# Kernel optimization log

Hardware: AMD Instinct MI355X
Metric: run time of the kernel (lower is better)

## Reference

```python
import jax, jax.numpy as jnp
import numpy as np

NUM_LAYERS = 3
HIDDEN = 128
EDGE_CH = 4
VOCAB = 100
N_NODES = 100000
N_EDGES = 600000


def setup_inputs() -> dict:
    key = jax.random.key(0)
    ks = jax.random.split(key, 10)
    z = jax.random.randint(ks[0], (N_NODES,), 0, VOCAB)
    edge_index = jax.random.randint(ks[1], (2, N_EDGES), 0, N_NODES)
    edge_attr = jax.random.normal(ks[2], (N_EDGES, EDGE_CH), dtype=jnp.float32)
    batch_vec = jnp.sort(jax.random.randint(ks[3], (N_NODES,), 0, 512))
    s = 1.0 / np.sqrt(HIDDEN)
    emb = jax.random.normal(ks[4], (VOCAB, HIDDEN), dtype=jnp.float32)
    We = jax.random.normal(ks[5], (NUM_LAYERS, EDGE_CH, HIDDEN), dtype=jnp.float32) * 0.5
    be = jnp.zeros((NUM_LAYERS, HIDDEN), dtype=jnp.float32)
    W1 = jax.random.normal(ks[6], (NUM_LAYERS, HIDDEN, HIDDEN), dtype=jnp.float32) * s
    b1 = jnp.zeros((NUM_LAYERS, HIDDEN), dtype=jnp.float32)
    W2 = jax.random.normal(ks[7], (NUM_LAYERS, HIDDEN, HIDDEN), dtype=jnp.float32) * s
    b2 = jnp.zeros((NUM_LAYERS, HIDDEN), dtype=jnp.float32)
    return {"emb": emb, "We": We, "be": be, "W1": W1, "b1": b1,
            "W2": W2, "b2": b2, "edge_attr": edge_attr,
            "z": z, "edge_index": edge_index, "batch_vec": batch_vec}


def reference(emb, We, be, W1, b1, W2, b2, edge_attr, z, edge_index, batch_vec):
    # atom embedding lookup: [N, H]
    x = emb[z]
    src, dst = edge_index[0], edge_index[1]
    n = x.shape[0]
    for l in range(NUM_LAYERS):
        # edge feature projection: [E, H]
        e = edge_attr @ We[l] + be[l]
        # GINE message: relu(x_j + e_ij), gather over src nodes
        m = jax.nn.relu(x[src] + e)
        # scatter-sum aggregation to destination nodes
        agg = jax.ops.segment_sum(m, dst, num_segments=n)
        # (1 + eps) * x + agg, eps = 0, then 2-layer MLP with silu act
        h = x + agg
        x = jax.nn.silu(h @ W1[l] + b1[l]) @ W2[l] + b2[l]
    return (x, batch_vec)
```

## Files before the change

kernel.cpp:

```cpp
#include <hip/hip_runtime.h>
#include <hip/hip_fp16.h>
#include <math.h>

#define N_NODES 100000
#define N_EDGES 600000
#define HIDDEN 128
#define EDGE_CH 4
#define NUM_LAYERS 3
#define MLP_ROWS 64

#define SCAN_BLOCK 256
#define SCAN_GRID ((N_NODES + SCAN_BLOCK - 1) / SCAN_BLOCK)

#define HSTR 132
#define MLP3_TILES ((N_NODES + 127) / 128)
#define MLP3_GRID 256

typedef short bf16x8 __attribute__((ext_vector_type(8)));
typedef float f32x4  __attribute__((ext_vector_type(4)));

__device__ inline unsigned short f2bf(float x) {
    unsigned u = __float_as_uint(x);
    return (unsigned short)((u + 0x7fff + ((u >> 16) & 1)) >> 16);
}
__device__ inline float bf2f(unsigned short b) { return __uint_as_float(((unsigned)b) << 16); }

__device__ inline float4 h8tof4(uint2 u) {
    __half2 a = *reinterpret_cast<const __half2*>(&u.x);
    __half2 b = *reinterpret_cast<const __half2*>(&u.y);
    float2 fa = __half22float2(a);
    float2 fb = __half22float2(b);
    return make_float4(fa.x, fa.y, fb.x, fb.y);
}
__device__ inline uint2 f4toh8(float4 v) {
    __half2 a = __floats2half2_rn(v.x, v.y);
    __half2 b = __floats2half2_rn(v.z, v.w);
    uint2 u;
    u.x = *reinterpret_cast<unsigned*>(&a);
    u.y = *reinterpret_cast<unsigned*>(&b);
    return u;
}


__global__ void embed_init_kernel(const float* __restrict__ emb,
                                  const int* __restrict__ z,
                                  float* __restrict__ x,
                                  float* __restrict__ agg,
                                  int write_agg,
                                  __half* __restrict__ xh,
                                  int write_xh) {
    int t = blockIdx.x * blockDim.x + threadIdx.x;
    int node = t >> 5;
    int c4 = t & 31;
    if (node < N_NODES) {
        float4 v = ((const float4*)(emb + (size_t)z[node] * HIDDEN))[c4];
        ((float4*)(x + (size_t)node * HIDDEN))[c4] = v;
        if (write_agg)
            ((float4*)(agg + (size_t)node * HIDDEN))[c4] = v;
        if (write_xh)
            ((uint2*)(xh + (size_t)node * HIDDEN))[c4] = f4toh8(v);
    }
}

__global__ void wprep_kernel(const float* __restrict__ W1, const float* __restrict__ W2,
                             unsigned short* __restrict__ wt) {
    int idx = blockIdx.x * blockDim.x + threadIdx.x;
    if (idx >= NUM_LAYERS * 2 * HIDDEN * HIDDEN) return;
    int j    = idx & 7;
    int lane = (idx >> 3) & 63;
    int ks   = (idx >> 9) & 3;
    int nt   = (idx >> 11) & 7;
    int mat  = (idx >> 14) & 1;
    int l    = idx >> 15;
    int n = nt * 16 + (lane & 15);
    int k = ks * 32 + (lane >> 4) * 8 + j;
    const float* W = mat ? W2 : W1;
    wt[idx] = f2bf(W[(size_t)l * HIDDEN * HIDDEN + (size_t)k * HIDDEN + n]);
}

__global__ __launch_bounds__(512, 1) void mlp_mfma3_kernel(
        const float* __restrict__ h,
        const unsigned short* __restrict__ wfrag,
        const float* __restrict__ b1, const float* __restrict__ b2,
        float* __restrict__ x,
        __half* __restrict__ xh,
        int write_xh) {
    __shared__ short wlds[2 * 16384];
    __shared__ float tbuf[8 * 16 * HSTR];
    int tid   = threadIdx.x;
    int wave  = tid >> 6;
    int lane  = tid & 63;
    int row16 = lane & 15;
    int quad  = lane >> 4;
    float* myt = tbuf + wave * 16 * HSTR;

    for (int i = tid; i < 4096; i += 512)
        ((float4*)wlds)[i] = ((const float4*)wfrag)[i];
    __syncthreads();

    float bias1[8], bias2[8];
    #pragma unroll
    for (int nt = 0; nt < 8; nt++) {
        bias1[nt] = b1[nt * 16 + row16];
        bias2[nt] = b2[nt * 16 + row16];
    }

    for (int tile = blockIdx.x; tile < MLP3_TILES; tile += gridDim.x) {
        int wnode0 = tile * 128 + wave * 16;
        int mnode  = wnode0 + row16;
        bool valid = (mnode < N_NODES);
        const float* hrow = h + (size_t)(valid ? mnode : 0) * HIDDEN + quad * 8;

        bf16x8 ahi[4], alo[4];
        #pragma unroll
        for (int ks = 0; ks < 4; ks++) {
            float v[8];
            *(float4*)(v + 0) = valid ? *(const float4*)(hrow + ks * 32 + 0) : make_float4(0.f,0.f,0.f,0.f);
            *(float4*)(v + 4) = valid ? *(const float4*)(hrow + ks * 32 + 4) : make_float4(0.f,0.f,0.f,0.f);
            bf16x8 hi, lo;
            #pragma unroll
            for (int j = 0; j < 8; j++) {
                unsigned short hb = f2bf(v[j]);
                hi[j] = (short)hb;
                lo[j] = (short)f2bf(v[j] - bf2f(hb));
            }
            ahi[ks] = hi; alo[ks] = lo;
        }

        f32x4 acc[8];
        #pragma unroll
        for (int nt = 0; nt < 8; nt++) acc[nt] = (f32x4){0.f, 0.f, 0.f, 0.f};
        #pragma unroll
        for (int ks = 0; ks < 4; ks++) {
            #pragma unroll
            for (int nt = 0; nt < 8; nt++) {
                bf16x8 Bv = *(const bf16x8*)(wlds + (size_t)((nt * 4 + ks) * 64 + lane) * 8);
                acc[nt] = __builtin_amdgcn_mfma_f32_16x16x32_bf16(ahi[ks], Bv, acc[nt], 0, 0, 0);
                acc[nt] = __builtin_amdgcn_mfma_f32_16x16x32_bf16(alo[ks], Bv, acc[nt], 0, 0, 0);
            }
        }

        #pragma unroll
        for (int nt = 0; nt < 8; nt++) {
            #pragma unroll
            for (int r = 0; r < 4; r++) {
                float v = acc[nt][r] + bias1[nt];
                v = v / (1.f + __expf(-v));
                myt[(quad * 4 + r) * HSTR + nt * 16 + row16] = v;
            }
        }

        #pragma unroll
        for (int ks = 0; ks < 4; ks++) {
            const float* p = myt + row16 * HSTR + ks * 32 + quad * 8;
            float v[8];
            *(float4*)(v + 0) = *(const float4*)(p + 0);
            *(float4*)(v + 4) = *(const float4*)(p + 4);
            bf16x8 hi, lo;
            #pragma unroll
            for (int j = 0; j < 8; j++) {
                unsigned short hb = f2bf(v[j]);
                hi[j] = (short)hb;
                lo[j] = (short)f2bf(v[j] - bf2f(hb));
            }
            ahi[ks] = hi; alo[ks] = lo;
        }

        #pragma unroll
        for (int nt = 0; nt < 8; nt++) acc[nt] = (f32x4){0.f, 0.f, 0.f, 0.f};
        #pragma unroll
        for (int ks = 0; ks < 4; ks++) {
            #pragma unroll
            for (int nt = 0; nt < 8; nt++) {
                bf16x8 Bv = *(const bf16x8*)(wlds + (size_t)(16384 + ((nt * 4 + ks) * 64 + lane) * 8));
                acc[nt] = __builtin_amdgcn_mfma_f32_16x16x32_bf16(ahi[ks], Bv, acc[nt], 0, 0, 0);
                acc[nt] = __builtin_amdgcn_mfma_f32_16x16x32_bf16(alo[ks], Bv, acc[nt], 0, 0, 0);
            }
        }

        #pragma unroll
        for (int nt = 0; nt < 8; nt++) {
            #pragma unroll
            for (int r = 0; r < 4; r++) {
                int node = wnode0 + quad * 4 + r;
                if (node < N_NODES) {
                    float v = acc[nt][r] + bias2[nt];
                    x[(size_t)node * HIDDEN + nt * 16 + row16] = v;
                    if (write_xh)
                        xh[(size_t)node * HIDDEN + nt * 16 + row16] = __float2half_rn(v);
                }
            }
        }
    }
}

__global__ void mlp_kernel(const float* __restrict__ h,
                           const float* __restrict__ W1, const float* __restrict__ b1,
                           const float* __restrict__ W2, const float* __restrict__ b2,
                           float* __restrict__ x) {
    __shared__ float hs[MLP_ROWS * HIDDEN];
    int rg = threadIdx.x >> 5;
    int c4 = threadIdx.x & 31;
    int node0 = blockIdx.x * MLP_ROWS;

    for (int i = threadIdx.x; i < MLP_ROWS * 32; i += 256) {
        int node = node0 + (i >> 5);
        float4 v = (node < N_NODES)
                 ? ((const float4*)(h + (size_t)node * HIDDEN))[i & 31]
                 : make_float4(0.f, 0.f, 0.f, 0.f);
        ((float4*)hs)[i] = v;
    }
    __syncthreads();

    float4 acc[8];
    {
        float4 bv = ((const float4*)b1)[c4];
        #pragma unroll
        for (int r = 0; r < 8; r++) acc[r] = bv;
    }
    const float* hbase = hs + rg * 8 * HIDDEN;

    for (int k4 = 0; k4 < HIDDEN; k4 += 4) {
        float4 w0 = ((const float4*)(W1 + (size_t)(k4 + 0) * HIDDEN))[c4];
        float4 w1 = ((const float4*)(W1 + (size_t)(k4 + 1) * HIDDEN))[c4];
        float4 w2 = ((const float4*)(W1 + (size_t)(k4 + 2) * HIDDEN))[c4];
        float4 w3 = ((const float4*)(W1 + (size_t)(k4 + 3) * HIDDEN))[c4];
        #pragma unroll
        for (int r = 0; r < 8; r++) {
            float4 hv = *(const float4*)(hbase + r * HIDDEN + k4);
            acc[r].x += hv.x*w0.x + hv.y*w1.x + hv.z*w2.x + hv.w*w3.x;
            acc[r].y += hv.x*w0.y + hv.y*w1.y + hv.z*w2.y + hv.w*w3.y;
            acc[r].z += hv.x*w0.z + hv.y*w1.z + hv.z*w2.z + hv.w*w3.z;
            acc[r].w += hv.x*w0.w + hv.y*w1.w + hv.z*w2.w + hv.w*w3.w;
        }
    }

    __syncthreads();
    #pragma unroll
    for (int r = 0; r < 8; r++) {
        float4 a = acc[r];
        a.x = a.x / (1.f + __expf(-a.x));
        a.y = a.y / (1.f + __expf(-a.y));
        a.z = a.z / (1.f + __expf(-a.z));
        a.w = a.w / (1.f + __expf(-a.w));
        *(float4*)(hs + (rg * 8 + r) * HIDDEN + c4 * 4) = a;
    }
    __syncthreads();

    {
        float4 bv = ((const float4*)b2)[c4];
        #pragma unroll
        for (int r = 0; r < 8; r++) acc[r] = bv;
    }
    for (int k4 = 0; k4 < HIDDEN; k4 += 4) {
        float4 w0 = ((const float4*)(W2 + (size_t)(k4 + 0) * HIDDEN))[c4];
        float4 w1 = ((const float4*)(W2 + (size_t)(k4 + 1) * HIDDEN))[c4];
        float4 w2 = ((const float4*)(W2 + (size_t)(k4 + 2) * HIDDEN))[c4];
        float4 w3 = ((const float4*)(W2 + (size_t)(k4 + 3) * HIDDEN))[c4];
        #pragma unroll
        for (int r = 0; r < 8; r++) {
            float4 hv = *(const float4*)(hbase + r * HIDDEN + k4);
            acc[r].x += hv.x*w0.x + hv.y*w1.x + hv.z*w2.x + hv.w*w3.x;
            acc[r].y += hv.x*w0.y + hv.y*w1.y + hv.z*w2.y + hv.w*w3.y;
            acc[r].z += hv.x*w0.z + hv.y*w1.z + hv.z*w2.z + hv.w*w3.z;
            acc[r].w += hv.x*w0.w + hv.y*w1.w + hv.z*w2.w + hv.w*w3.w;
        }
    }

    #pragma unroll
    for (int r = 0; r < 8; r++) {
        int node = node0 + rg * 8 + r;
        if (node < N_NODES)
            ((float4*)(x + (size_t)node * HIDDEN))[c4] = acc[r];
    }
}

__global__ void batch_out_kernel(const int* __restrict__ bv, float* __restrict__ out) {
    int i = blockIdx.x * blockDim.x + threadIdx.x;
    if (i < N_NODES) out[i] = (float)bv[i];
}


__global__ void zero_kernel(int* __restrict__ p, int n) {
    int i = blockIdx.x * blockDim.x + threadIdx.x;
    if (i < n) p[i] = 0;
}

__global__ void hist_kernel(const int* __restrict__ dst, int* __restrict__ cnt) {
    int e = blockIdx.x * blockDim.x + threadIdx.x;
    if (e < N_EDGES) atomicAdd(&cnt[dst[e]], 1);
}

__global__ void scan_partial_kernel(const int* __restrict__ cnt, int* __restrict__ bsum) {
    __shared__ int s[SCAN_BLOCK];
    int i = blockIdx.x * SCAN_BLOCK + threadIdx.x;
    s[threadIdx.x] = (i < N_NODES) ? cnt[i] : 0;
    __syncthreads();
    for (int off = SCAN_BLOCK / 2; off > 0; off >>= 1) {
        if (threadIdx.x < off) s[threadIdx.x] += s[threadIdx.x + off];
        __syncthreads();
    }
    if (threadIdx.x == 0) bsum[blockIdx.x] = s[0];
}

__global__ void scan_base_kernel(int* __restrict__ bsum) {
    __shared__ int s[512];
    int t = threadIdx.x;
    s[t] = (t < SCAN_GRID) ? bsum[t] : 0;
    __syncthreads();
    for (int off = 1; off < 512; off <<= 1) {
        int v = (t >= off) ? s[t - off] : 0;
        __syncthreads();
        s[t] += v;
        __syncthreads();
    }
    if (t < SCAN_GRID) bsum[t] = (t > 0) ? s[t - 1] : 0;
}

__global__ void scan_final_kernel(int* __restrict__ cnt, const int* __restrict__ bsum) {
    __shared__ int s[SCAN_BLOCK];
    int i = blockIdx.x * SCAN_BLOCK + threadIdx.x;
    int v = (i < N_NODES) ? cnt[i] : 0;
    s[threadIdx.x] = v;
    __syncthreads();
    for (int off = 1; off < SCAN_BLOCK; off <<= 1) {
        int u = (threadIdx.x >= off) ? s[threadIdx.x - off] : 0;
        __syncthreads();
        s[threadIdx.x] += u;
        __syncthreads();
    }
    if (i < N_NODES) cnt[i] = bsum[blockIdx.x] + s[threadIdx.x] - v;
}

__global__ void scatter2_kernel(const int* __restrict__ dst,
                                const int* __restrict__ src,
                                const float* __restrict__ edge_attr,
                                int* __restrict__ pos,
                                int* __restrict__ ssrc,
                                float4* __restrict__ sea) {
    int e = blockIdx.x * blockDim.x + threadIdx.x;
    if (e < N_EDGES) {
        int p = atomicAdd(&pos[dst[e]], 1);
        ssrc[p] = src[e];
        sea[p] = ((const float4*)edge_attr)[e];
    }
}

__global__ void gather2_kernel(const float* __restrict__ x,
                               const int* __restrict__ ssrc,
                               const float4* __restrict__ sea,
                               const int* __restrict__ pos,
                               const float* __restrict__ We_l,
                               const float* __restrict__ be_l,
                               float* __restrict__ h) {
    __shared__ float sWe[EDGE_CH * HIDDEN];
    __shared__ float sbe[HIDDEN];
    for (int i = threadIdx.x; i < EDGE_CH * HIDDEN; i += blockDim.x) sWe[i] = We_l[i];
    if (threadIdx.x < HIDDEN) sbe[threadIdx.x] = be_l[threadIdx.x];
    __syncthreads();

    int t = blockIdx.x * blockDim.x + threadIdx.x;
    int node = t >> 5;
    int c4 = t & 31;
    if (node >= N_NODES) return;

    int start = (node == 0) ? 0 : pos[node - 1];
    int end = pos[node];

    float4 w0 = ((const float4*)sWe)[0 * 32 + c4];
    float4 w1 = ((const float4*)sWe)[1 * 32 + c4];
    float4 w2 = ((const float4*)sWe)[2 * 32 + c4];
    float4 w3 = ((const float4*)sWe)[3 * 32 + c4];
    float4 bb = ((const float4*)sbe)[c4];

    float4 acc = make_float4(0.f, 0.f, 0.f, 0.f);
    int j = start;
    if (j < end) {
        int s0 = ssrc[j];
        float4 ea0 = sea[j];
        for (; j + 1 < end; j++) {
            int s1 = ssrc[j + 1];
            float4 ea1 = sea[j + 1];
            float4 xv = ((const float4*)(x + (size_t)s0 * HIDDEN))[c4];
            float m0 = xv.x + ea0.x*w0.x + ea0.y*w1.x + ea0.z*w2.x + ea0.w*w3.x + bb.x;
            float m1 = xv.y + ea0.x*w0.y + ea0.y*w1.y + ea0.z*w2.y + ea0.w*w3.y + bb.y;
            float m2 = xv.z + ea0.x*w0.z + ea0.y*w1.z + ea0.z*w2.z + ea0.w*w3.z + bb.z;
            float m3 = xv.w + ea0.x*w0.w + ea0.y*w1.w + ea0.z*w2.w + ea0.w*w3.w + bb.w;
            acc.x += fmaxf(m0, 0.f); acc.y += fmaxf(m1, 0.f);
            acc.z += fmaxf(m2, 0.f); acc.w += fmaxf(m3, 0.f);
            s0 = s1; ea0 = ea1;
        }
        float4 xv = ((const float4*)(x + (size_t)s0 * HIDDEN))[c4];
        float m0 = xv.x + ea0.x*w0.x + ea0.y*w1.x + ea0.z*w2.x + ea0.w*w3.x + bb.x;
        float m1 = xv.y + ea0.x*w0.y + ea0.y*w1.y + ea0.z*w2.y + ea0.w*w3.y + bb.y;
        float m2 = xv.z + ea0.x*w0.z + ea0.y*w1.z + ea0.z*w2.z + ea0.w*w3.z + bb.z;
        float m3 = xv.w + ea0.x*w0.w + ea0.y*w1.w + ea0.z*w2.w + ea0.w*w3.w + bb.w;
        acc.x += fmaxf(m0, 0.f); acc.y += fmaxf(m1, 0.f);
        acc.z += fmaxf(m2, 0.f); acc.w += fmaxf(m3, 0.f);
    }
    float4 xi = ((const float4*)(x + (size_t)node * HIDDEN))[c4];
    acc.x += xi.x; acc.y += xi.y; acc.z += xi.z; acc.w += xi.w;
    ((float4*)(h + (size_t)node * HIDDEN))[c4] = acc;
}

__global__ void gather3_kernel(const __half* __restrict__ xh,
                               const int* __restrict__ ssrc,
                               const float4* __restrict__ sea,
                               const int* __restrict__ pos,
                               const float* __restrict__ We_l,
                               const float* __restrict__ be_l,
                               float* __restrict__ h) {
    __shared__ float sWe[EDGE_CH * HIDDEN];
    __shared__ float sbe[HIDDEN];
    for (int i = threadIdx.x; i < EDGE_CH * HIDDEN; i += blockDim.x) sWe[i] = We_l[i];
    if (threadIdx.x < HIDDEN) sbe[threadIdx.x] = be_l[threadIdx.x];
    __syncthreads();

    int t = blockIdx.x * blockDim.x + threadIdx.x;
    int node = t >> 5;
    int c4 = t & 31;
    if (node >= N_NODES) return;

    int start = (node == 0) ? 0 : pos[node - 1];
    int end = pos[node];

    float4 w0 = ((const float4*)sWe)[0 * 32 + c4];
    float4 w1 = ((const float4*)sWe)[1 * 32 + c4];
    float4 w2 = ((const float4*)sWe)[2 * 32 + c4];
    float4 w3 = ((const float4*)sWe)[3 * 32 + c4];
    float4 bb = ((const float4*)sbe)[c4];

    float4 acc = make_float4(0.f, 0.f, 0.f, 0.f);
    int j = start;
    if (j < end) {
        int s0 = ssrc[j];
        float4 ea0 = sea[j];
        for (; j + 1 < end; j++) {
            int s1 = ssrc[j + 1];
            float4 ea1 = sea[j + 1];
            float4 xv = h8tof4(((const uint2*)(xh + (size_t)s0 * HIDDEN))[c4]);
            float m0 = xv.x + ea0.x*w0.x + ea0.y*w1.x + ea0.z*w2.x + ea0.w*w3.x + bb.x;
            float m1 = xv.y + ea0.x*w0.y + ea0.y*w1.y + ea0.z*w2.y + ea0.w*w3.y + bb.y;
            float m2 = xv.z + ea0.x*w0.z + ea0.y*w1.z + ea0.z*w2.z + ea0.w*w3.z + bb.z;
            float m3 = xv.w + ea0.x*w0.w + ea0.y*w1.w + ea0.z*w2.w + ea0.w*w3.w + bb.w;
            acc.x += fmaxf(m0, 0.f); acc.y += fmaxf(m1, 0.f);
            acc.z += fmaxf(m2, 0.f); acc.w += fmaxf(m3, 0.f);
            s0 = s1; ea0 = ea1;
        }
        float4 xv = h8tof4(((const uint2*)(xh + (size_t)s0 * HIDDEN))[c4]);
        float m0 = xv.x + ea0.x*w0.x + ea0.y*w1.x + ea0.z*w2.x + ea0.w*w3.x + bb.x;
        float m1 = xv.y + ea0.x*w0.y + ea0.y*w1.y + ea0.z*w2.y + ea0.w*w3.y + bb.y;
        float m2 = xv.z + ea0.x*w0.z + ea0.y*w1.z + ea0.z*w2.z + ea0.w*w3.z + bb.z;
        float m3 = xv.w + ea0.x*w0.w + ea0.y*w1.w + ea0.z*w2.w + ea0.w*w3.w + bb.w;
        acc.x += fmaxf(m0, 0.f); acc.y += fmaxf(m1, 0.f);
        acc.z += fmaxf(m2, 0.f); acc.w += fmaxf(m3, 0.f);
    }
    float4 xi = h8tof4(((const uint2*)(xh + (size_t)node * HIDDEN))[c4]);
    acc.x += xi.x; acc.y += xi.y; acc.z += xi.z; acc.w += xi.w;
    ((float4*)(h + (size_t)node * HIDDEN))[c4] = acc;
}


__global__ void edge_kernel(const float* __restrict__ x,
                            const float* __restrict__ edge_attr,
                            const int* __restrict__ src,
                            const int* __restrict__ dst,
                            const float* __restrict__ We_l,
                            const float* __restrict__ be_l,
                            float* __restrict__ agg) {
    __shared__ float sWe[EDGE_CH * HIDDEN];
    __shared__ float sbe[HIDDEN];
    for (int i = threadIdx.x; i < EDGE_CH * HIDDEN; i += blockDim.x) sWe[i] = We_l[i];
    if (threadIdx.x < HIDDEN) sbe[threadIdx.x] = be_l[threadIdx.x];
    __syncthreads();

    int t = blockIdx.x * blockDim.x + threadIdx.x;
    int e = t >> 5;
    if (e >= N_EDGES) return;
    int c4 = t & 31;

    int s = src[e];
    int d = dst[e];
    float4 ea = ((const float4*)edge_attr)[e];
    float4 w0 = ((const float4*)sWe)[0 * 32 + c4];
    float4 w1 = ((const float4*)sWe)[1 * 32 + c4];
    float4 w2 = ((const float4*)sWe)[2 * 32 + c4];
    float4 w3 = ((const float4*)sWe)[3 * 32 + c4];
    float4 bb = ((const float4*)sbe)[c4];
    float4 xv = ((const float4*)(x + (size_t)s * HIDDEN))[c4];

    float m0 = xv.x + ea.x*w0.x + ea.y*w1.x + ea.z*w2.x + ea.w*w3.x + bb.x;
    float m1 = xv.y + ea.x*w0.y + ea.y*w1.y + ea.z*w2.y + ea.w*w3.y + bb.y;
    float m2 = xv.z + ea.x*w0.z + ea.y*w1.z + ea.z*w2.z + ea.w*w3.z + bb.z;
    float m3 = xv.w + ea.x*w0.w + ea.y*w1.w + ea.z*w2.w + ea.w*w3.w + bb.w;

    float* ap = agg + (size_t)d * HIDDEN + c4 * 4;
    atomicAdd(ap + 0, fmaxf(m0, 0.f));
    atomicAdd(ap + 1, fmaxf(m1, 0.f));
    atomicAdd(ap + 2, fmaxf(m2, 0.f));
    atomicAdd(ap + 3, fmaxf(m3, 0.f));
}


extern "C" void kernel_launch(void* const* d_in, const int* in_sizes, int n_in,
                              void* d_out, int out_size, void* d_ws, size_t ws_size,
                              hipStream_t stream) {
    const float* emb       = (const float*)d_in[0];
    const float* We        = (const float*)d_in[1];
    const float* be        = (const float*)d_in[2];
    const float* W1        = (const float*)d_in[3];
    const float* b1        = (const float*)d_in[4];
    const float* W2        = (const float*)d_in[5];
    const float* b2        = (const float*)d_in[6];
    const float* edge_attr = (const float*)d_in[7];
    const int*   z         = (const int*)d_in[8];
    const int*   ei        = (const int*)d_in[9];
    const int*   bv        = (const int*)d_in[10];

    float* x   = (float*)d_out;
    float* agg = (float*)d_ws;
    const int* src = ei;
    const int* dst = ei + N_EDGES;

    const size_t AGG_BYTES  = (size_t)N_NODES * HIDDEN * sizeof(float);
    const size_t POS_BYTES  = (size_t)N_NODES * sizeof(int);
    const size_t SRC_BYTES  = (size_t)N_EDGES * sizeof(int);
    const size_t EA_BYTES   = (size_t)N_EDGES * 4 * sizeof(float);
    const size_t BSUM_BYTES = ((size_t)SCAN_GRID * sizeof(int) + 15) & ~15;
    const size_t WT_ELEMS   = (size_t)NUM_LAYERS * 2 * HIDDEN * HIDDEN;
    const size_t WT_BYTES   = WT_ELEMS * sizeof(unsigned short);
    const size_t XH_BYTES   = (size_t)N_NODES * HIDDEN * sizeof(__half);

    const size_t OFF_POS  = AGG_BYTES;
    const size_t OFF_SRC  = OFF_POS + POS_BYTES;
    const size_t OFF_EA   = OFF_SRC + SRC_BYTES;
    const size_t OFF_BSUM = OFF_EA + EA_BYTES;
    const size_t OFF_WT   = OFF_BSUM + BSUM_BYTES;
    const size_t OFF_XH   = OFF_WT + WT_BYTES;
    const size_t TOTAL    = OFF_WT + WT_BYTES;
    const size_t TOTAL2   = OFF_XH + XH_BYTES;

    const int MLP_GRID = (N_NODES + MLP_ROWS - 1) / MLP_ROWS;

    if (ws_size >= OFF_BSUM + BSUM_BYTES) {
        int*    pos  = (int*)((char*)d_ws + OFF_POS);
        int*    ssrc = (int*)((char*)d_ws + OFF_SRC);
        float4* sea  = (float4*)((char*)d_ws + OFF_EA);
        int*    bsum = (int*)((char*)d_ws + OFF_BSUM);
        const bool mfma  = (ws_size >= TOTAL);
        const bool halfx = (ws_size >= TOTAL2);
        unsigned short* wt = (unsigned short*)((char*)d_ws + OFF_WT);
        __half* xh = (__half*)((char*)d_ws + OFF_XH);

        embed_init_kernel<<<(N_NODES * 32) / 256, 256, 0, stream>>>(
            emb, z, x, agg, 0, xh, halfx ? 1 : 0);
        zero_kernel<<<(N_NODES + 255) / 256, 256, 0, stream>>>(pos, N_NODES);
        hist_kernel<<<(N_EDGES + 255) / 256, 256, 0, stream>>>(dst, pos);
        scan_partial_kernel<<<SCAN_GRID, SCAN_BLOCK, 0, stream>>>(pos, bsum);
        scan_base_kernel<<<1, 512, 0, stream>>>(bsum);
        scan_final_kernel<<<SCAN_GRID, SCAN_BLOCK, 0, stream>>>(pos, bsum);
        scatter2_kernel<<<(N_EDGES + 255) / 256, 256, 0, stream>>>(dst, src, edge_attr, pos, ssrc, sea);
        if (mfma)
            wprep_kernel<<<((int)WT_ELEMS + 255) / 256, 256, 0, stream>>>(W1, W2, wt);

        for (int l = 0; l < NUM_LAYERS; l++) {
            if (halfx) {
                gather3_kernel<<<(N_NODES * 32 + 255) / 256, 256, 0, stream>>>(
                    xh, ssrc, sea, pos,
                    We + (size_t)l * EDGE_CH * HIDDEN, be + (size_t)l * HIDDEN, agg);
            } else {
                gather2_kernel<<<(N_NODES * 32 + 255) / 256, 256, 0, stream>>>(
                    x, ssrc, sea, pos,
                    We + (size_t)l * EDGE_CH * HIDDEN, be + (size_t)l * HIDDEN, agg);
            }
            if (mfma) {
                int wxh = (halfx && l < NUM_LAYERS - 1) ? 1 : 0;
                mlp_mfma3_kernel<<<MLP3_GRID, 512, 0, stream>>>(
                    agg,
                    wt + (size_t)(l * 2) * HIDDEN * HIDDEN,
                    b1 + (size_t)l * HIDDEN, b2 + (size_t)l * HIDDEN, x, xh, wxh);
            } else {
                mlp_kernel<<<MLP_GRID, 256, 0, stream>>>(
                    agg,
                    W1 + (size_t)l * HIDDEN * HIDDEN, b1 + (size_t)l * HIDDEN,
                    W2 + (size_t)l * HIDDEN * HIDDEN, b2 + (size_t)l * HIDDEN, x);
            }
        }
    } else {
        embed_init_kernel<<<(N_NODES * 32) / 256, 256, 0, stream>>>(
            emb, z, x, agg, 1, (__half*)nullptr, 0);
        for (int l = 0; l < NUM_LAYERS; l++) {
            edge_kernel<<<(N_EDGES * 32) / 256, 256, 0, stream>>>(
                x, edge_attr, src, dst,
                We + (size_t)l * EDGE_CH * HIDDEN, be + (size_t)l * HIDDEN, agg);
            mlp_kernel<<<MLP_GRID, 256, 0, stream>>>(
                agg,
                W1 + (size_t)l * HIDDEN * HIDDEN, b1 + (size_t)l * HIDDEN,
                W2 + (size_t)l * HIDDEN * HIDDEN, b2 + (size_t)l * HIDDEN, x);
        }
    }

    batch_out_kernel<<<(N_NODES + 255) / 256, 256, 0, stream>>>(bv, x + (size_t)N_NODES * HIDDEN);
}
```

Baseline: 432.3 us.

## Shrink MLP kernel LDS footprint for higher occupancy and skip redundant fp32 x writes

The fused MLP kernel now uses 256-thread blocks with 64-node tiles and keeps only W1 fragments in LDS. W2 fragments are read from global memory (likely L2-cached), and the SiLU intermediate is staged through LDS in two 64-column halves, so both the weight buffer and the scratch buffer shrink. This is meant to allow three blocks per CU instead of one, improving latency hiding. Separately, fp32 x is no longer written by the embedding step or by intermediate layers when the half-precision copy feeds the next gather, which cuts store traffic. The cost is that W2 loads now go to global/L2 memory instead of LDS.

```diff
diff --git a/kernel.cpp b/kernel.cpp
--- a/kernel.cpp
+++ b/kernel.cpp
@@ -12,9 +12,9 @@
 #define SCAN_BLOCK 256
 #define SCAN_GRID ((N_NODES + SCAN_BLOCK - 1) / SCAN_BLOCK)
 
-#define HSTR 132
-#define MLP3_TILES ((N_NODES + 127) / 128)
-#define MLP3_GRID 256
+#define TSTR 68
+#define MLP4_TILES ((N_NODES + 63) / 64)
+#define MLP4_GRID 768
 
 typedef short bf16x8 __attribute__((ext_vector_type(8)));
 typedef float f32x4  __attribute__((ext_vector_type(4)));
@@ -48,13 +48,15 @@
                                   float* __restrict__ agg,
                                   int write_agg,
                                   __half* __restrict__ xh,
-                                  int write_xh) {
+                                  int write_xh,
+                                  int write_x) {
     int t = blockIdx.x * blockDim.x + threadIdx.x;
     int node = t >> 5;
     int c4 = t & 31;
     if (node < N_NODES) {
         float4 v = ((const float4*)(emb + (size_t)z[node] * HIDDEN))[c4];
-        ((float4*)(x + (size_t)node * HIDDEN))[c4] = v;
+        if (write_x)
+            ((float4*)(x + (size_t)node * HIDDEN))[c4] = v;
         if (write_agg)
             ((float4*)(agg + (size_t)node * HIDDEN))[c4] = v;
         if (write_xh)
@@ -78,23 +80,24 @@
     wt[idx] = f2bf(W[(size_t)l * HIDDEN * HIDDEN + (size_t)k * HIDDEN + n]);
 }
 
-__global__ __launch_bounds__(512, 1) void mlp_mfma3_kernel(
+__global__ __launch_bounds__(256, 3) void mlp_mfma4_kernel(
         const float* __restrict__ h,
         const unsigned short* __restrict__ wfrag,
         const float* __restrict__ b1, const float* __restrict__ b2,
         float* __restrict__ x,
         __half* __restrict__ xh,
-        int write_xh) {
-    __shared__ short wlds[2 * 16384];
-    __shared__ float tbuf[8 * 16 * HSTR];
+        int write_x, int write_xh) {
+    __shared__ short wlds[16384];
+    __shared__ float tbuf[4 * 16 * TSTR];
     int tid   = threadIdx.x;
     int wave  = tid >> 6;
     int lane  = tid & 63;
     int row16 = lane & 15;
     int quad  = lane >> 4;
-    float* myt = tbuf + wave * 16 * HSTR;
-
-    for (int i = tid; i < 4096; i += 512)
+    float* myt = tbuf + wave * 16 * TSTR;
+    const unsigned short* w2g = wfrag + 16384;
+
+    for (int i = tid; i < 2048; i += 256)
         ((float4*)wlds)[i] = ((const float4*)wfrag)[i];
     __syncthreads();
 
@@ -105,8 +108,8 @@
         bias2[nt] = b2[nt * 16 + row16];
     }
 
-    for (int tile = blockIdx.x; tile < MLP3_TILES; tile += gridDim.x) {
-        int wnode0 = tile * 128 + wave * 16;
+    for (int tile = blockIdx.x; tile < MLP4_TILES; tile += gridDim.x) {
+        int wnode0 = tile * 64 + wave * 16;
         int mnode  = wnode0 + row16;
         bool valid = (mnode < N_NODES);
         const float* hrow = h + (size_t)(valid ? mnode : 0) * HIDDEN + quad * 8;
@@ -127,54 +130,62 @@
             ahi[ks] = hi; alo[ks] = lo;
         }
 
-        f32x4 acc[8];
-        #pragma unroll
-        for (int nt = 0; nt < 8; nt++) acc[nt] = (f32x4){0.f, 0.f, 0.f, 0.f};
+        f32x4 acc1[8];
+        #pragma unroll
+        for (int nt = 0; nt < 8; nt++) acc1[nt] = (f32x4){0.f, 0.f, 0.f, 0.f};
         #pragma unroll
         for (int ks = 0; ks < 4; ks++) {
             #pragma unroll
             for (int nt = 0; nt < 8; nt++) {
                 bf16x8 Bv = *(const bf16x8*)(wlds + (size_t)((nt * 4 + ks) * 64 + lane) * 8);
-                acc[nt] = __builtin_amdgcn_mfma_f32_16x16x32_bf16(ahi[ks], Bv, acc[nt], 0, 0, 0);
-                acc[nt] = __builtin_amdgcn_mfma_f32_16x16x32_bf16(alo[ks], Bv, acc[nt], 0, 0, 0);
-            }
-        }
-
-        #pragma unroll
-        for (int nt = 0; nt < 8; nt++) {
+                acc1[nt] = __builtin_amdgcn_mfma_f32_16x16x32_bf16(ahi[ks], Bv, acc1[nt], 0, 0, 0);
+                acc1[nt] = __builtin_amdgcn_mfma_f32_16x16x32_bf16(alo[ks], Bv, acc1[nt], 0, 0, 0);
+            }
+        }
+
+        f32x4 acc2[8];
+        #pragma unroll
+        for (int nt = 0; nt < 8; nt++) acc2[nt] = (f32x4){0.f, 0.f, 0.f, 0.f};
+
+        #pragma unroll
+        for (int p = 0; p < 2; p++) {
             #pragma unroll
-            for (int r = 0; r < 4; r++) {
-                float v = acc[nt][r] + bias1[nt];
-                v = v / (1.f + __expf(-v));
-                myt[(quad * 4 + r) * HSTR + nt * 16 + row16] = v;
-            }
-        }
-
-        #pragma unroll
-        for (int ks = 0; ks < 4; ks++) {
-            const float* p = myt + row16 * HSTR + ks * 32 + quad * 8;
-            float v[8];
-            *(float4*)(v + 0) = *(const float4*)(p + 0);
-            *(float4*)(v + 4) = *(const float4*)(p + 4);
-            bf16x8 hi, lo;
+            for (int l4 = 0; l4 < 4; l4++) {
+                int nt = p * 4 + l4;
+                #pragma unroll
+                for (int r = 0; r < 4; r++) {
+                    float v = acc1[nt][r] + bias1[nt];
+                    v = v / (1.f + __expf(-v));
+                    myt[(quad * 4 + r) * TSTR + l4 * 16 + row16] = v;
+                }
+            }
+
+            bf16x8 a2hi[2], a2lo[2];
             #pragma unroll
-            for (int j = 0; j < 8; j++) {
-                unsigned short hb = f2bf(v[j]);
-                hi[j] = (short)hb;
-                lo[j] = (short)f2bf(v[j] - bf2f(hb));
-            }
-            ahi[ks] = hi; alo[ks] = lo;
-        }
-
-        #pragma unroll
-        for (int nt = 0; nt < 8; nt++) acc[nt] = (f32x4){0.f, 0.f, 0.f, 0.f};
-        #pragma unroll
-        for (int ks = 0; ks < 4; ks++) {
+            for (int kk = 0; kk < 2; kk++) {
+                const float* pp = myt + row16 * TSTR + kk * 32 + quad * 8;
+                float v[8];
+                *(float4*)(v + 0) = *(const float4*)(pp + 0);
+                *(float4*)(v + 4) = *(const float4*)(pp + 4);
+                bf16x8 hi, lo;
+                #pragma unroll
+                for (int j = 0; j < 8; j++) {
+                    unsigned short hb = f2bf(v[j]);
+                    hi[j] = (short)hb;
+                    lo[j] = (short)f2bf(v[j] - bf2f(hb));
+                }
+                a2hi[kk] = hi; a2lo[kk] = lo;
+            }
+
             #pragma unroll
-            for (int nt = 0; nt < 8; nt++) {
-                bf16x8 Bv = *(const bf16x8*)(wlds + (size_t)(16384 + ((nt * 4 + ks) * 64 + lane) * 8));
-                acc[nt] = __builtin_amdgcn_mfma_f32_16x16x32_bf16(ahi[ks], Bv, acc[nt], 0, 0, 0);
-                acc[nt] = __builtin_amdgcn_mfma_f32_16x16x32_bf16(alo[ks], Bv, acc[nt], 0, 0, 0);
+            for (int kk = 0; kk < 2; kk++) {
+                int ks = p * 2 + kk;
+                #pragma unroll
+                for (int nt = 0; nt < 8; nt++) {
+                    bf16x8 Bv = *(const bf16x8*)(w2g + (size_t)((nt * 4 + ks) * 64 + lane) * 8);
+                    acc2[nt] = __builtin_amdgcn_mfma_f32_16x16x32_bf16(a2hi[kk], Bv, acc2[nt], 0, 0, 0);
+                    acc2[nt] = __builtin_amdgcn_mfma_f32_16x16x32_bf16(a2lo[kk], Bv, acc2[nt], 0, 0, 0);
+                }
             }
         }
 
@@ -184,8 +195,9 @@
             for (int r = 0; r < 4; r++) {
                 int node = wnode0 + quad * 4 + r;
                 if (node < N_NODES) {
-                    float v = acc[nt][r] + bias2[nt];
-                    x[(size_t)node * HIDDEN + nt * 16 + row16] = v;
+                    float v = acc2[nt][r] + bias2[nt];
+                    if (write_x)
+                        x[(size_t)node * HIDDEN + nt * 16 + row16] = v;
                     if (write_xh)
                         xh[(size_t)node * HIDDEN + nt * 16 + row16] = __float2half_rn(v);
                 }
@@ -553,7 +565,7 @@
         __half* xh = (__half*)((char*)d_ws + OFF_XH);
 
         embed_init_kernel<<<(N_NODES * 32) / 256, 256, 0, stream>>>(
-            emb, z, x, agg, 0, xh, halfx ? 1 : 0);
+            emb, z, x, agg, 0, xh, halfx ? 1 : 0, halfx ? 0 : 1);
         zero_kernel<<<(N_NODES + 255) / 256, 256, 0, stream>>>(pos, N_NODES);
         hist_kernel<<<(N_EDGES + 255) / 256, 256, 0, stream>>>(dst, pos);
         scan_partial_kernel<<<SCAN_GRID, SCAN_BLOCK, 0, stream>>>(pos, bsum);
@@ -574,11 +586,12 @@
                     We + (size_t)l * EDGE_CH * HIDDEN, be + (size_t)l * HIDDEN, agg);
             }
             if (mfma) {
+                int wx  = (!halfx || l == NUM_LAYERS - 1) ? 1 : 0;
                 int wxh = (halfx && l < NUM_LAYERS - 1) ? 1 : 0;
-                mlp_mfma3_kernel<<<MLP3_GRID, 512, 0, stream>>>(
+                mlp_mfma4_kernel<<<MLP4_GRID, 256, 0, stream>>>(
                     agg,
                     wt + (size_t)(l * 2) * HIDDEN * HIDDEN,
-                    b1 + (size_t)l * HIDDEN, b2 + (size_t)l * HIDDEN, x, xh, wxh);
+                    b1 + (size_t)l * HIDDEN, b2 + (size_t)l * HIDDEN, x, xh, wx, wxh);
             } else {
                 mlp_kernel<<<MLP_GRID, 256, 0, stream>>>(
                     agg,
@@ -588,7 +601,7 @@
         }
     } else {
         embed_init_kernel<<<(N_NODES * 32) / 256, 256, 0, stream>>>(
-            emb, z, x, agg, 1, (__half*)nullptr, 0);
+            emb, z, x, agg, 1, (__half*)nullptr, 0, 1);
         for (int l = 0; l < NUM_LAYERS; l++) {
             edge_kernel<<<(N_EDGES * 32) / 256, 256, 0, stream>>>(
                 x, edge_attr, src, dst,
```

New measurement: 487.7 us. 1.13x slower.
